# Kernel optimization log

Hardware: AMD Instinct MI355X
Metric: run time of the kernel (lower is better)

Reference implementation:

```python
import jax, jax.numpy as jnp
import numpy as np

N_NODES = 50000
N_EDGES = 1600000
NUM_MP_STEPS = 6


def _init_linear(key, d_in, d_out):
    kw, kb = jax.random.split(key)
    lim = 1.0 / np.sqrt(d_in)
    W = jax.random.uniform(kw, (d_in, d_out), jnp.float32, -lim, lim)
    b = jax.random.uniform(kb, (d_out,), jnp.float32, -lim, lim)
    return W, b


def setup_inputs() -> dict:
    key = jax.random.key(0)
    ks = jax.random.split(key, 12)
    inp = {
        'x': jax.random.normal(ks[0], (N_NODES, 32), jnp.float32),
        'edge_index': jax.random.randint(ks[1], (2, N_EDGES), 0, N_NODES, jnp.int64),
        'edge_attr': jax.random.normal(ks[2], (N_EDGES, 6), jnp.float32),
    }
    # encoder edge MLP: 6 -> 18 -> 18 -> 16 (leaky relu after every layer)
    inp['enc_W0'], inp['enc_b0'] = _init_linear(ks[3], 6, 18)
    inp['enc_W1'], inp['enc_b1'] = _init_linear(ks[4], 18, 18)
    inp['enc_W2'], inp['enc_b2'] = _init_linear(ks[5], 18, 16)
    # edge model MLP: 160 -> 80 -> 16 (leaky relu)
    inp['edge_W0'], inp['edge_b0'] = _init_linear(ks[6], 160, 80)
    inp['edge_W1'], inp['edge_b1'] = _init_linear(ks[7], 80, 16)
    # node model MLP: 80 -> 56 -> 32 (plain relu: MPGraph does not pass use_leaky_relu here)
    inp['node_W0'], inp['node_b0'] = _init_linear(ks[8], 80, 56)
    inp['node_W1'], inp['node_b1'] = _init_linear(ks[9], 56, 32)
    return inp


def reference(x, edge_index, edge_attr,
              enc_W0, enc_b0, enc_W1, enc_b1, enc_W2, enc_b2,
              edge_W0, edge_b0, edge_W1, edge_b1,
              node_W0, node_b0, node_W1, node_b1):
    lrelu = jax.nn.leaky_relu  # negative_slope=0.01, matches nn.LeakyReLU()
    relu = jax.nn.relu
    row, col = edge_index[0], edge_index[1]
    n_nodes = x.shape[0]

    # encoder on edge feats, LeakyReLU on node feats
    e = lrelu(lrelu(lrelu(edge_attr @ enc_W0 + enc_b0) @ enc_W1 + enc_b1) @ enc_W2 + enc_b2)
    n = lrelu(x)
    e0, n0 = e, n

    ones_e = jnp.ones((row.shape[0], 1), x.dtype)
    outputs = []
    for step in range(1, NUM_MP_STEPS + 1):
        ec = jnp.concatenate([e0, e], axis=1)            # [E, 32] reattach initial edges
        nc = jnp.concatenate([n0, n], axis=1)            # [N, 64] reattach initial nodes
        # edge update: gather endpoints, concat, MLP
        eh = jnp.concatenate([nc[row], nc[col], ec], axis=1)   # [E, 160]
        e = lrelu(lrelu(eh @ edge_W0 + edge_b0) @ edge_W1 + edge_b1)  # [E, 16]
        # node update: scatter-mean messages to source nodes, concat, MLP
        s = jax.ops.segment_sum(e, row, num_segments=n_nodes)         # [N, 16]
        cnt = jax.ops.segment_sum(ones_e, row, num_segments=n_nodes)  # [N, 1]
        msg = s / jnp.maximum(cnt, 1.0)
        nh = jnp.concatenate([nc, msg], axis=1)                        # [N, 80]
        n = relu(relu(nh @ node_W0 + node_b0) @ node_W1 + node_b1)     # [N, 32]
        if step > 1:
            outputs.append(e)
    return tuple(outputs)
```

## Files before the change

### kernel.cpp

```cpp
#include <hip/hip_runtime.h>

#define N_NODES 50000
#define N_EDGES 1600000

#define O_ENCW0 0
#define O_ENCB0 108
#define O_ENCW1 126
#define O_ENCB1 450
#define O_ENCW2 468
#define O_ENCB2 756
#define O_EDGEW0 772
#define O_EDGEB0 13572
#define O_EDGEW1 13652
#define O_EDGEB1 14932
#define O_NODEW0 14948
#define O_NODEB0 19428
#define O_NODEW1 19484
#define O_NODEB1 21276
#define W_TOTAL 21308

typedef __attribute__((ext_vector_type(8))) short bf16x8;
typedef __attribute__((ext_vector_type(4))) short bf16x4;
typedef __attribute__((ext_vector_type(4))) float f32x4;

__device__ __forceinline__ float bf2f(unsigned int u) {
    return __uint_as_float(u << 16);
}
__device__ __forceinline__ unsigned short f2bf(float f) {
    unsigned int u = __float_as_uint(f);
    u += 0x7fffu + ((u >> 16) & 1u);
    return (unsigned short)(u >> 16);
}
__device__ __forceinline__ float lrelu(float x) { return x > 0.f ? x : 0.01f * x; }

__device__ __forceinline__ bf16x8 pack8(float4 a, float4 b) {
    bf16x8 r;
    r[0] = (short)f2bf(a.x); r[1] = (short)f2bf(a.y);
    r[2] = (short)f2bf(a.z); r[3] = (short)f2bf(a.w);
    r[4] = (short)f2bf(b.x); r[5] = (short)f2bf(b.y);
    r[6] = (short)f2bf(b.z); r[7] = (short)f2bf(b.w);
    return r;
}

struct WPack {
    const float* p[14];
    int off[15];
};

__global__ void detect_flags(const int* __restrict__ eidx, int* __restrict__ flags) {
    int t = threadIdx.x;
    int v = eidx[2 * t + 1];
    unsigned long long bi = __ballot(v != 0);
    if (t == 0) flags[0] = (bi == 0ull) ? 1 : 0;
}

__device__ __forceinline__ void load_rc(const int* eidx, int flag64, int e, int& r, int& c) {
    if (flag64) {
        const long long* e64 = (const long long*)eidx;
        r = (int)e64[e];
        c = (int)e64[N_EDGES + e];
    } else {
        r = eidx[e];
        c = eidx[N_EDGES + e];
    }
}
__device__ __forceinline__ int load_r(const int* eidx, int flag64, int e) {
    return flag64 ? (int)((const long long*)eidx)[e] : eidx[e];
}

__global__ void copy_w(WPack P, float* __restrict__ dst) {
    int a = blockIdx.x;
    const float* s = P.p[a];
    int n = P.off[a + 1] - P.off[a];
    float* d = dst + P.off[a];
    for (int i = threadIdx.x; i < n; i += 256) d[i] = s[i];
}

__global__ void build_wT(const float* __restrict__ w0,
                         const float* __restrict__ w1,
                         unsigned short* __restrict__ wT) {
    int t = blockIdx.x * 256 + threadIdx.x;
    if (t < 12800) {
        int col = t / 160, k = t % 160;
        wT[t] = f2bf(w0[k * 80 + col]);
    } else if (t < 14336) {
        int u = t - 12800;
        int col = u / 96, k = u % 96;
        wT[t] = (k < 80) ? f2bf(w1[k * 16 + col]) : (unsigned short)0;
    }
}

__global__ void __launch_bounds__(256) init_nodes(const float* __restrict__ x,
                                                  unsigned short* __restrict__ ncb,
                                                  int* __restrict__ cnti) {
    int i = blockIdx.x * 256 + threadIdx.x;
    if (i >= N_NODES) return;
    const float4* xin = (const float4*)(x + (size_t)i * 32);
    uint4* np = (uint4*)(ncb + (size_t)i * 64);
#pragma unroll
    for (int q = 0; q < 4; q++) {
        float4 a = xin[2 * q];
        float4 b = xin[2 * q + 1];
        unsigned int w0 = (unsigned int)f2bf(lrelu(a.x)) | ((unsigned int)f2bf(lrelu(a.y)) << 16);
        unsigned int w1 = (unsigned int)f2bf(lrelu(a.z)) | ((unsigned int)f2bf(lrelu(a.w)) << 16);
        unsigned int w2 = (unsigned int)f2bf(lrelu(b.x)) | ((unsigned int)f2bf(lrelu(b.y)) << 16);
        unsigned int w3 = (unsigned int)f2bf(lrelu(b.z)) | ((unsigned int)f2bf(lrelu(b.w)) << 16);
        uint4 o = make_uint4(w0, w1, w2, w3);
        np[q] = o;
        np[4 + q] = o;
    }
    cnti[i] = 0;
}

__global__ void count_edges(const int* __restrict__ eidx, const int* __restrict__ flags,
                            int* __restrict__ cnti) {
    int e = blockIdx.x * 256 + threadIdx.x;
    atomicAdd(&cnti[load_r(eidx, flags[0], e)], 1);
}

__global__ void __launch_bounds__(256) scan_offsets(const int* __restrict__ cnti,
                                                    int* __restrict__ off,
                                                    int* __restrict__ cursor) {
    __shared__ int ls[256];
    const int t = threadIdx.x;
    const int lo = t * 196;
    const int hi = min(lo + 196, N_NODES);
    int sum = 0;
    for (int i = lo; i < hi; i++) sum += cnti[i];
    ls[t] = sum;
    __syncthreads();
    for (int d = 1; d < 256; d <<= 1) {
        int v = (t >= d) ? ls[t - d] : 0;
        __syncthreads();
        ls[t] += v;
        __syncthreads();
    }
    int run = (t == 0) ? 0 : ls[t - 1];
    for (int i = lo; i < hi; i++) {
        off[i] = run;
        cursor[i] = run;
        run += cnti[i];
    }
    if (t == 255) off[N_NODES] = run;
}

template <int EXT>
__global__ void build_perm(const int* __restrict__ eidx, const int* __restrict__ flags,
                           int* __restrict__ cursor, int* __restrict__ perm,
                           int2* __restrict__ rcp, int* __restrict__ pose) {
    int e = blockIdx.x * 256 + threadIdx.x;
    int r, c;
    load_rc(eidx, flags[0], e, r, c);
    int pos = atomicAdd(&cursor[r], 1);
    perm[pos] = e;
    if (EXT) {
        rcp[pos] = make_int2(r, c);
        pose[e] = pos;
    }
}

template <int MODE>
__global__ void __launch_bounds__(256) encoder(const float* __restrict__ ea,
                                               const float* __restrict__ wsW,
                                               float* __restrict__ outbase,
                                               unsigned short* __restrict__ e0b,
                                               const int* __restrict__ pose) {
    int e = blockIdx.x * 256 + threadIdx.x;
    const float* ap = ea + (size_t)e * 6;
    float a[6];
#pragma unroll
    for (int k = 0; k < 6; k++) a[k] = ap[k];

    float h1[18];
#pragma unroll
    for (int j = 0; j < 18; j++) h1[j] = wsW[O_ENCB0 + j];
#pragma unroll
    for (int k = 0; k < 6; k++) {
        float v = a[k];
#pragma unroll
        for (int j = 0; j < 18; j++) h1[j] = fmaf(v, wsW[O_ENCW0 + k * 18 + j], h1[j]);
    }
#pragma unroll
    for (int j = 0; j < 18; j++) h1[j] = lrelu(h1[j]);

    float h2[18];
#pragma unroll
    for (int j = 0; j < 18; j++) h2[j] = wsW[O_ENCB1 + j];
#pragma unroll
    for (int k = 0; k < 18; k++) {
        float v = h1[k];
#pragma unroll
        for (int j = 0; j < 18; j++) h2[j] = fmaf(v, wsW[O_ENCW1 + k * 18 + j], h2[j]);
    }
#pragma unroll
    for (int j = 0; j < 18; j++) h2[j] = lrelu(h2[j]);

    float o[16];
#pragma unroll
    for (int j = 0; j < 16; j++) o[j] = wsW[O_ENCB2 + j];
#pragma unroll
    for (int k = 0; k < 18; k++) {
        float v = h2[k];
#pragma unroll
        for (int j = 0; j < 16; j++) o[j] = fmaf(v, wsW[O_ENCW2 + k * 16 + j], o[j]);
    }
    if (MODE == 0) {
        float4* ow = (float4*)(outbase + (size_t)4 * N_EDGES * 16 + (size_t)e * 16);
#pragma unroll
        for (int q = 0; q < 4; q++)
            ow[q] = make_float4(lrelu(o[4 * q]), lrelu(o[4 * q + 1]),
                                lrelu(o[4 * q + 2]), lrelu(o[4 * q + 3]));
    } else {
        unsigned int pw[8];
#pragma unroll
        for (int q = 0; q < 8; q++) {
            float a0 = lrelu(o[2 * q]), a1 = lrelu(o[2 * q + 1]);
            pw[q] = (unsigned int)f2bf(a0) | ((unsigned int)f2bf(a1) << 16);
        }
        size_t pos = (MODE == 2) ? (size_t)pose[e] : (size_t)e;
        uint4* ow = (uint4*)(e0b + pos * 16);
        ow[0] = make_uint4(pw[0], pw[1], pw[2], pw[3]);
        ow[1] = make_uint4(pw[4], pw[5], pw[6], pw[7]);
    }
}


__global__ void __launch_bounds__(256) edge_mfma(const unsigned short* __restrict__ ncb,
                                                 const float* __restrict__ outb_c,
                                                 int slot_e0, int slot_prev, int slot_cur,
                                                 const int* __restrict__ eidx,
                                                 const int* __restrict__ flags,
                                                 const float* __restrict__ wsW,
                                                 const unsigned short* __restrict__ wT,
                                                 float* __restrict__ outb) {
    __shared__ unsigned short act1[4][32 * 104];
    const int lane = threadIdx.x & 63;
    const int wave = threadIdx.x >> 6;
    const int r16 = lane & 15;
    const int g = lane >> 4;
    const int flag64 = flags[0];
    unsigned short* aw = act1[wave];

    const int ebase = blockIdx.x * 128 + wave * 32;
    const float* e0s = outb_c + (size_t)slot_e0 * N_EDGES * 16;
    const float* eps = outb_c + (size_t)slot_prev * N_EDGES * 16;

#pragma unroll
    for (int u = 0; u < 2; u++) {
        bf16x4 z4 = {0, 0, 0, 0};
        *(bf16x4*)&aw[(u * 16 + r16) * 104 + 80 + g * 4] = z4;
    }

    bf16x8 a[2][5];
#pragma unroll
    for (int u = 0; u < 2; u++) {
        const int el = ebase + u * 16 + r16;
        int r_el, c_el;
        load_rc(eidx, flag64, el, r_el, c_el);
        a[u][0] = *(const bf16x8*)(ncb + (size_t)r_el * 64 + g * 8);
        a[u][1] = *(const bf16x8*)(ncb + (size_t)r_el * 64 + 32 + g * 8);
        a[u][2] = *(const bf16x8*)(ncb + (size_t)c_el * 64 + g * 8);
        a[u][3] = *(const bf16x8*)(ncb + (size_t)c_el * 64 + 32 + g * 8);
        const float* src = (g < 2) ? e0s : eps;
        const float4* p = (const float4*)(src + (size_t)el * 16 + (g & 1) * 8);
        a[u][4] = pack8(p[0], p[1]);
    }

#pragma unroll
    for (int t = 0; t < 5; t++) {
        float bv = wsW[O_EDGEB0 + t * 16 + r16];
        f32x4 acc0 = {bv, bv, bv, bv};
        f32x4 acc1 = {bv, bv, bv, bv};
#pragma unroll
        for (int st = 0; st < 5; st++) {
            bf16x8 b = *(const bf16x8*)(wT + (t * 16 + r16) * 160 + st * 32 + g * 8);
            acc0 = __builtin_amdgcn_mfma_f32_16x16x32_bf16(a[0][st], b, acc0, 0, 0, 0);
            acc1 = __builtin_amdgcn_mfma_f32_16x16x32_bf16(a[1][st], b, acc1, 0, 0, 0);
        }
#pragma unroll
        for (int i = 0; i < 4; i++) {
            aw[(g * 4 + i) * 104 + t * 16 + r16]      = f2bf(lrelu(acc0[i]));
            aw[(16 + g * 4 + i) * 104 + t * 16 + r16] = f2bf(lrelu(acc1[i]));
        }
    }
    asm volatile("s_waitcnt lgkmcnt(0)" ::: "memory");
    __builtin_amdgcn_sched_barrier(0);

    float bv2 = wsW[O_EDGEB1 + r16];
    f32x4 acc20 = {bv2, bv2, bv2, bv2};
    f32x4 acc21 = {bv2, bv2, bv2, bv2};
#pragma unroll
    for (int st = 0; st < 3; st++) {
        bf16x8 b2 = *(const bf16x8*)(wT + 12800 + r16 * 96 + st * 32 + g * 8);
        bf16x8 a20 = *(const bf16x8*)&aw[r16 * 104 + st * 32 + g * 8];
        bf16x8 a21 = *(const bf16x8*)&aw[(16 + r16) * 104 + st * 32 + g * 8];
        acc20 = __builtin_amdgcn_mfma_f32_16x16x32_bf16(a20, b2, acc20, 0, 0, 0);
        acc21 = __builtin_amdgcn_mfma_f32_16x16x32_bf16(a21, b2, acc21, 0, 0, 0);
    }

    float* oc = outb + (size_t)slot_cur * N_EDGES * 16;
#pragma unroll
    for (int i = 0; i < 4; i++) {
        int eg0 = ebase + g * 4 + i;
        int eg1 = ebase + 16 + g * 4 + i;
        oc[(size_t)eg0 * 16 + r16] = lrelu(acc20[i]);
        oc[(size_t)eg1 * 16 + r16] = lrelu(acc21[i]);
    }
}

template <int WOUT>
__global__ void __launch_bounds__(256) edge_mfma_b16(const unsigned short* __restrict__ ncb,
                                                     const unsigned short* __restrict__ e0b,
                                                     const unsigned short* __restrict__ prevb,
                                                     unsigned short* __restrict__ curb,
                                                     const int* __restrict__ eidx,
                                                     const int* __restrict__ flags,
                                                     const float* __restrict__ wsW,
                                                     const unsigned short* __restrict__ wT,
                                                     float* __restrict__ oc) {
    __shared__ unsigned short act1[4][32 * 104];
    const int lane = threadIdx.x & 63;
    const int wave = threadIdx.x >> 6;
    const int r16 = lane & 15;
    const int g = lane >> 4;
    const int flag64 = flags[0];
    unsigned short* aw = act1[wave];

    const int ebase = blockIdx.x * 128 + wave * 32;

#pragma unroll
    for (int u = 0; u < 2; u++) {
        bf16x4 z4 = {0, 0, 0, 0};
        *(bf16x4*)&aw[(u * 16 + r16) * 104 + 80 + g * 4] = z4;
    }

    bf16x8 a[2][5];
#pragma unroll
    for (int u = 0; u < 2; u++) {
        const int el = ebase + u * 16 + r16;
        int r_el, c_el;
        load_rc(eidx, flag64, el, r_el, c_el);
        a[u][0] = *(const bf16x8*)(ncb + (size_t)r_el * 64 + g * 8);
        a[u][1] = *(const bf16x8*)(ncb + (size_t)r_el * 64 + 32 + g * 8);
        a[u][2] = *(const bf16x8*)(ncb + (size_t)c_el * 64 + g * 8);
        a[u][3] = *(const bf16x8*)(ncb + (size_t)c_el * 64 + 32 + g * 8);
        const unsigned short* src = (g < 2) ? e0b : prevb;
        a[u][4] = *(const bf16x8*)(src + (size_t)el * 16 + (g & 1) * 8);
    }

#pragma unroll
    for (int t = 0; t < 5; t++) {
        float bv = wsW[O_EDGEB0 + t * 16 + r16];
        f32x4 acc0 = {bv, bv, bv, bv};
        f32x4 acc1 = {bv, bv, bv, bv};
#pragma unroll
        for (int st = 0; st < 5; st++) {
            bf16x8 b = *(const bf16x8*)(wT + (t * 16 + r16) * 160 + st * 32 + g * 8);
            acc0 = __builtin_amdgcn_mfma_f32_16x16x32_bf16(a[0][st], b, acc0, 0, 0, 0);
            acc1 = __builtin_amdgcn_mfma_f32_16x16x32_bf16(a[1][st], b, acc1, 0, 0, 0);
        }
#pragma unroll
        for (int i = 0; i < 4; i++) {
            aw[(g * 4 + i) * 104 + t * 16 + r16]      = f2bf(lrelu(acc0[i]));
            aw[(16 + g * 4 + i) * 104 + t * 16 + r16] = f2bf(lrelu(acc1[i]));
        }
    }
    asm volatile("s_waitcnt lgkmcnt(0)" ::: "memory");
    __builtin_amdgcn_sched_barrier(0);

    float bv2 = wsW[O_EDGEB1 + r16];
    f32x4 acc20 = {bv2, bv2, bv2, bv2};
    f32x4 acc21 = {bv2, bv2, bv2, bv2};
#pragma unroll
    for (int st = 0; st < 3; st++) {
        bf16x8 b2 = *(const bf16x8*)(wT + 12800 + r16 * 96 + st * 32 + g * 8);
        bf16x8 a20 = *(const bf16x8*)&aw[r16 * 104 + st * 32 + g * 8];
        bf16x8 a21 = *(const bf16x8*)&aw[(16 + r16) * 104 + st * 32 + g * 8];
        acc20 = __builtin_amdgcn_mfma_f32_16x16x32_bf16(a20, b2, acc20, 0, 0, 0);
        acc21 = __builtin_amdgcn_mfma_f32_16x16x32_bf16(a21, b2, acc21, 0, 0, 0);
    }

#pragma unroll
    for (int i = 0; i < 4; i++) {
        int eg0 = ebase + g * 4 + i;
        int eg1 = ebase + 16 + g * 4 + i;
        float v0 = lrelu(acc20[i]);
        float v1 = lrelu(acc21[i]);
        curb[(size_t)eg0 * 16 + r16] = f2bf(v0);
        curb[(size_t)eg1 * 16 + r16] = f2bf(v1);
        if (WOUT) {
            oc[(size_t)eg0 * 16 + r16] = v0;
            oc[(size_t)eg1 * 16 + r16] = v1;
        }
    }
}

template <int WOUT>
__global__ void __launch_bounds__(256) edge_mfma_perm(const unsigned short* __restrict__ ncb,
                                                      const unsigned short* __restrict__ e0b,
                                                      const unsigned short* __restrict__ prevb,
                                                      unsigned short* __restrict__ curb,
                                                      const int2* __restrict__ rcp,
                                                      const int* __restrict__ perm,
                                                      const float* __restrict__ wsW,
                                                      const unsigned short* __restrict__ wT,
                                                      float* __restrict__ oc) {
    __shared__ unsigned short act1[4][32 * 104];
    const int lane = threadIdx.x & 63;
    const int wave = threadIdx.x >> 6;
    const int r16 = lane & 15;
    const int g = lane >> 4;
    unsigned short* aw = act1[wave];

    const int pbase = blockIdx.x * 128 + wave * 32;

#pragma unroll
    for (int u = 0; u < 2; u++) {
        bf16x4 z4 = {0, 0, 0, 0};
        *(bf16x4*)&aw[(u * 16 + r16) * 104 + 80 + g * 4] = z4;
    }

    bf16x8 a[2][5];
#pragma unroll
    for (int u = 0; u < 2; u++) {
        const int pl = pbase + u * 16 + r16;
        int2 rc = rcp[pl];
        a[u][0] = *(const bf16x8*)(ncb + (size_t)rc.x * 64 + g * 8);
        a[u][1] = *(const bf16x8*)(ncb + (size_t)rc.x * 64 + 32 + g * 8);
        a[u][2] = *(const bf16x8*)(ncb + (size_t)rc.y * 64 + g * 8);
        a[u][3] = *(const bf16x8*)(ncb + (size_t)rc.y * 64 + 32 + g * 8);
        const unsigned short* src = (g < 2) ? e0b : prevb;
        a[u][4] = *(const bf16x8*)(src + (size_t)pl * 16 + (g & 1) * 8);
    }

#pragma unroll
    for (int t = 0; t < 5; t++) {
        float bv = wsW[O_EDGEB0 + t * 16 + r16];
        f32x4 acc0 = {bv, bv, bv, bv};
        f32x4 acc1 = {bv, bv, bv, bv};
#pragma unroll
        for (int st = 0; st < 5; st++) {
            bf16x8 b = *(const bf16x8*)(wT + (t * 16 + r16) * 160 + st * 32 + g * 8);
            acc0 = __builtin_amdgcn_mfma_f32_16x16x32_bf16(a[0][st], b, acc0, 0, 0, 0);
            acc1 = __builtin_amdgcn_mfma_f32_16x16x32_bf16(a[1][st], b, acc1, 0, 0, 0);
        }
#pragma unroll
        for (int i = 0; i < 4; i++) {
            aw[(g * 4 + i) * 104 + t * 16 + r16]      = f2bf(lrelu(acc0[i]));
            aw[(16 + g * 4 + i) * 104 + t * 16 + r16] = f2bf(lrelu(acc1[i]));
        }
    }
    asm volatile("s_waitcnt lgkmcnt(0)" ::: "memory");
    __builtin_amdgcn_sched_barrier(0);

    float bv2 = wsW[O_EDGEB1 + r16];
    f32x4 acc20 = {bv2, bv2, bv2, bv2};
    f32x4 acc21 = {bv2, bv2, bv2, bv2};
#pragma unroll
    for (int st = 0; st < 3; st++) {
        bf16x8 b2 = *(const bf16x8*)(wT + 12800 + r16 * 96 + st * 32 + g * 8);
        bf16x8 a20 = *(const bf16x8*)&aw[r16 * 104 + st * 32 + g * 8];
        bf16x8 a21 = *(const bf16x8*)&aw[(16 + r16) * 104 + st * 32 + g * 8];
        acc20 = __builtin_amdgcn_mfma_f32_16x16x32_bf16(a20, b2, acc20, 0, 0, 0);
        acc21 = __builtin_amdgcn_mfma_f32_16x16x32_bf16(a21, b2, acc21, 0, 0, 0);
    }

#pragma unroll
    for (int i = 0; i < 4; i++) {
        int p0l = pbase + g * 4 + i;
        int p1l = pbase + 16 + g * 4 + i;
        float v0 = lrelu(acc20[i]);
        float v1 = lrelu(acc21[i]);
        curb[(size_t)p0l * 16 + r16] = f2bf(v0);
        curb[(size_t)p1l * 16 + r16] = f2bf(v1);
        if (WOUT) {
            int eo0 = perm[p0l];
            int eo1 = perm[p1l];
            oc[(size_t)eo0 * 16 + r16] = v0;
            oc[(size_t)eo1 * 16 + r16] = v1;
        }
    }
}

__global__ void __launch_bounds__(256) gather_mean(const int* __restrict__ off,
                                                   const int* __restrict__ perm,
                                                   const float* __restrict__ ecur,
                                                   float* __restrict__ msg) {
    const int wave = threadIdx.x >> 6;
    const int lane = threadIdx.x & 63;
    const int i = blockIdx.x * 4 + wave;
    const int c = lane & 15;
    const int sub = lane >> 4;
    const int p0 = off[i], p1 = off[i + 1];
    float sum = 0.f;
    for (int p = p0 + sub; p < p1; p += 4)
        sum += ecur[(size_t)perm[p] * 16 + c];
    sum += __shfl_xor(sum, 16, 64);
    sum += __shfl_xor(sum, 32, 64);
    if (lane < 16) {
        float inv = 1.0f / fmaxf((float)(p1 - p0), 1.0f);
        msg[(size_t)i * 16 + c] = sum * inv;
    }
}

__global__ void __launch_bounds__(256) gather_mean_b16(const int* __restrict__ off,
                                                       const int* __restrict__ perm,
                                                       const unsigned short* __restrict__ ecurb,
                                                       float* __restrict__ msg) {
    const int wave = threadIdx.x >> 6;
    const int lane = threadIdx.x & 63;
    const int i = blockIdx.x * 4 + wave;
    const int c = lane & 15;
    const int sub = lane >> 4;
    const int p0 = off[i], p1 = off[i + 1];
    float sum = 0.f;
    for (int p = p0 + sub; p < p1; p += 4)
        sum += bf2f((unsigned int)ecurb[(size_t)perm[p] * 16 + c]);
    sum += __shfl_xor(sum, 16, 64);
    sum += __shfl_xor(sum, 32, 64);
    if (lane < 16) {
        float inv = 1.0f / fmaxf((float)(p1 - p0), 1.0f);
        msg[(size_t)i * 16 + c] = sum * inv;
    }
}

__global__ void __launch_bounds__(256) gather_mean_seq(const int* __restrict__ off,
                                                       const unsigned short* __restrict__ ecurb,
                                                       float* __restrict__ msg) {
    const int wave = threadIdx.x >> 6;
    const int lane = threadIdx.x & 63;
    const int i = blockIdx.x * 4 + wave;
    const int c = lane & 15;
    const int sub = lane >> 4;
    const int p0 = off[i], p1 = off[i + 1];
    float sum = 0.f;
    for (int p = p0 + sub; p < p1; p += 4)
        sum += bf2f((unsigned int)ecurb[(size_t)p * 16 + c]);
    sum += __shfl_xor(sum, 16, 64);
    sum += __shfl_xor(sum, 32, 64);
    if (lane < 16) {
        float inv = 1.0f / fmaxf((float)(p1 - p0), 1.0f);
        msg[(size_t)i * 16 + c] = sum * inv;
    }
}

__global__ void __launch_bounds__(64) node_mlp(const float* __restrict__ msg,
                                               unsigned short* __restrict__ ncb,
                                               const float* __restrict__ wsW) {
    __shared__ float sl[64 * 81];
    const int l = threadIdx.x;
    const int i = blockIdx.x * 64 + l;
    if (i >= N_NODES) return;
    const float* W0 = wsW + O_NODEW0;
    const float* b0 = wsW + O_NODEB0;
    const float* W1 = wsW + O_NODEW1;
    const float* b1 = wsW + O_NODEB1;

    const uint4* ncp = (const uint4*)(ncb + (size_t)i * 64);
#pragma unroll
    for (int q = 0; q < 8; q++) {
        uint4 u = ncp[q];
        int base = l * 81 + 8 * q;
        sl[base + 0] = bf2f(u.x & 0xffffu); sl[base + 1] = bf2f(u.x >> 16);
        sl[base + 2] = bf2f(u.y & 0xffffu); sl[base + 3] = bf2f(u.y >> 16);
        sl[base + 4] = bf2f(u.z & 0xffffu); sl[base + 5] = bf2f(u.z >> 16);
        sl[base + 6] = bf2f(u.w & 0xffffu); sl[base + 7] = bf2f(u.w >> 16);
    }
    const float4* mp = (const float4*)(msg + (size_t)i * 16);
#pragma unroll
    for (int q = 0; q < 4; q++) {
        float4 v = mp[q];
        int base = l * 81 + 64 + 4 * q;
        sl[base] = v.x; sl[base + 1] = v.y; sl[base + 2] = v.z; sl[base + 3] = v.w;
    }

    float h[56];
#pragma unroll
    for (int q = 0; q < 14; q++) {
        float4 b = ((const float4*)b0)[q];
        h[4 * q] = b.x; h[4 * q + 1] = b.y; h[4 * q + 2] = b.z; h[4 * q + 3] = b.w;
    }
    for (int k = 0; k < 80; k++) {
        float v = sl[l * 81 + k];
        const float4* w = (const float4*)(W0 + k * 56);
#pragma unroll
        for (int q = 0; q < 14; q++) {
            float4 wv = w[q];
            h[4 * q]     = fmaf(v, wv.x, h[4 * q]);
            h[4 * q + 1] = fmaf(v, wv.y, h[4 * q + 1]);
            h[4 * q + 2] = fmaf(v, wv.z, h[4 * q + 2]);
            h[4 * q + 3] = fmaf(v, wv.w, h[4 * q + 3]);
        }
    }
#pragma unroll
    for (int j = 0; j < 56; j++) sl[l * 81 + j] = fmaxf(h[j], 0.f);

    float o[32];
#pragma unroll
    for (int q = 0; q < 8; q++) {
        float4 b = ((const float4*)b1)[q];
        o[4 * q] = b.x; o[4 * q + 1] = b.y; o[4 * q + 2] = b.z; o[4 * q + 3] = b.w;
    }
    for (int j = 0; j < 56; j++) {
        float v = sl[l * 81 + j];
        const float4* w = (const float4*)(W1 + j * 32);
#pragma unroll
        for (int q = 0; q < 8; q++) {
            float4 wv = w[q];
            o[4 * q]     = fmaf(v, wv.x, o[4 * q]);
            o[4 * q + 1] = fmaf(v, wv.y, o[4 * q + 1]);
            o[4 * q + 2] = fmaf(v, wv.z, o[4 * q + 2]);
            o[4 * q + 3] = fmaf(v, wv.w, o[4 * q + 3]);
        }
    }
    uint4* nout = (uint4*)(ncb + (size_t)i * 64 + 32);
#pragma unroll
    for (int q = 0; q < 4; q++) {
        unsigned int w0 = (unsigned int)f2bf(fmaxf(o[8 * q + 0], 0.f)) |
                          ((unsigned int)f2bf(fmaxf(o[8 * q + 1], 0.f)) << 16);
        unsigned int w1 = (unsigned int)f2bf(fmaxf(o[8 * q + 2], 0.f)) |
                          ((unsigned int)f2bf(fmaxf(o[8 * q + 3], 0.f)) << 16);
        unsigned int w2 = (unsigned int)f2bf(fmaxf(o[8 * q + 4], 0.f)) |
                          ((unsigned int)f2bf(fmaxf(o[8 * q + 5], 0.f)) << 16);
        unsigned int w3 = (unsigned int)f2bf(fmaxf(o[8 * q + 6], 0.f)) |
                          ((unsigned int)f2bf(fmaxf(o[8 * q + 7], 0.f)) << 16);
        nout[q] = make_uint4(w0, w1, w2, w3);
    }
}

extern "C" void kernel_launch(void* const* d_in, const int* in_sizes, int n_in,
                              void* d_out, int out_size, void* d_ws, size_t ws_size,
                              hipStream_t stream) {
    (void)in_sizes; (void)n_in; (void)out_size;
    const float* x  = (const float*)d_in[0];
    const int* eidx = (const int*)d_in[1];
    const float* ea = (const float*)d_in[2];
    float* out = (float*)d_out;

    char* wsb = (char*)d_ws;
    float* wsW  = (float*)(wsb + 0);
    int* flags  = (int*)(wsb + 85232);
    int* cnti   = (int*)(wsb + 85248);
    int* off    = (int*)(wsb + 285248);
    int* cursor = (int*)(wsb + 485264);
    int* perm   = (int*)(wsb + 685264);
    unsigned short* ncb = (unsigned short*)(wsb + 7085264);
    unsigned short* wT  = (unsigned short*)(wsb + 13485264);
    float* msg  = (float*)(wsb + 13513936);
    const size_t WS_BASE = 16713936ull;
    unsigned short* e0b = (unsigned short*)(wsb + 16714240);
    unsigned short* rb0 = e0b + (size_t)N_EDGES * 16;
    unsigned short* rb1 = rb0 + (size_t)N_EDGES * 16;
    const size_t WS_BIG = 16714240ull + 3ull * 51200000ull;
    int2* rcp = (int2*)(wsb + 170314240ull);
    int* pose = (int*)(wsb + 183114240ull);
    const size_t WS_PERM = 189514240ull;
    if (ws_size < WS_BASE) return;
    const bool big  = (ws_size >= WS_BIG);
    const bool prm  = (ws_size >= WS_PERM);

    WPack P;
    static const int offs[15] = {0, 108, 126, 450, 468, 756, 772, 13572, 13652,
                                 14932, 14948, 19428, 19484, 21276, 21308};
    for (int a = 0; a < 14; a++) P.p[a] = (const float*)d_in[3 + a];
    for (int a = 0; a < 15; a++) P.off[a] = offs[a];

    detect_flags<<<1, 64, 0, stream>>>(eidx, flags);
    copy_w<<<14, 256, 0, stream>>>(P, wsW);
    build_wT<<<56, 256, 0, stream>>>((const float*)d_in[9], (const float*)d_in[11], wT);
    init_nodes<<<196, 256, 0, stream>>>(x, ncb, cnti);
    count_edges<<<N_EDGES / 256, 256, 0, stream>>>(eidx, flags, cnti);
    scan_offsets<<<1, 256, 0, stream>>>(cnti, off, cursor);
    if (prm)
        build_perm<1><<<N_EDGES / 256, 256, 0, stream>>>(eidx, flags, cursor, perm, rcp, pose);
    else
        build_perm<0><<<N_EDGES / 256, 256, 0, stream>>>(eidx, flags, cursor, perm, nullptr, nullptr);

    if (prm) {
        encoder<2><<<N_EDGES / 256, 256, 0, stream>>>(ea, wsW, out, e0b, pose);
        unsigned short* rings[2] = {rb0, rb1};
        for (int t = 1; t <= 6; t++) {
            unsigned short* prevb = (t == 1) ? e0b : rings[(t - 1) & 1];
            unsigned short* curb  = rings[t & 1];
            if (t == 1)
                edge_mfma_perm<0><<<N_EDGES / 128, 256, 0, stream>>>(
                    ncb, e0b, prevb, curb, rcp, perm, wsW, wT, out);
            else
                edge_mfma_perm<1><<<N_EDGES / 128, 256, 0, stream>>>(
                    ncb, e0b, prevb, curb, rcp, perm, wsW, wT,
                    out + (size_t)(t - 2) * N_EDGES * 16);
            if (t < 6) {
                gather_mean_seq<<<12500, 256, 0, stream>>>(off, curb, msg);
                node_mlp<<<782, 64, 0, stream>>>(msg, ncb, wsW);
            }
        }
    } else if (big) {
        encoder<1><<<N_EDGES / 256, 256, 0, stream>>>(ea, wsW, out, e0b, nullptr);
        unsigned short* rings[2] = {rb0, rb1};
        for (int t = 1; t <= 6; t++) {
            unsigned short* prevb = (t == 1) ? e0b : rings[(t - 1) & 1];
            unsigned short* curb  = rings[t & 1];
            if (t == 1)
                edge_mfma_b16<0><<<N_EDGES / 128, 256, 0, stream>>>(
                    ncb, e0b, prevb, curb, eidx, flags, wsW, wT, out);
            else
                edge_mfma_b16<1><<<N_EDGES / 128, 256, 0, stream>>>(
                    ncb, e0b, prevb, curb, eidx, flags, wsW, wT,
                    out + (size_t)(t - 2) * N_EDGES * 16);
            if (t < 6) {
                gather_mean_b16<<<12500, 256, 0, stream>>>(off, perm, curb, msg);
                node_mlp<<<782, 64, 0, stream>>>(msg, ncb, wsW);
            }
        }
    } else {
        encoder<0><<<N_EDGES / 256, 256, 0, stream>>>(ea, wsW, out, nullptr, nullptr);
        const int prevs[6] = {4, 0, 0, 1, 2, 3};
        const int curs[6]  = {0, 0, 1, 2, 3, 4};
        for (int t = 1; t <= 6; t++) {
            edge_mfma<<<N_EDGES / 128, 256, 0, stream>>>(ncb, out, 4, prevs[t - 1],
                                                         curs[t - 1], eidx, flags, wsW,
                                                         wT, out);
            if (t < 6) {
                gather_mean<<<12500, 256, 0, stream>>>(
                    off, perm, out + (size_t)curs[t - 1] * N_EDGES * 16, msg);
                node_mlp<<<782, 64, 0, stream>>>(msg, ncb, wsW);
            }
        }
    }
}
```

Measured before the change: 1.604 ms.

## Fuse segment-mean gather with node MLP using bf16 MFMA per 16-node wave tile

Replaces the separate gather_mean_seq and scalar node_mlp kernels with one node_fused kernel. Each wave gathers 16 nodes' features and mean messages into LDS, then runs both node MLP layers with 16x16x32 bf16 MFMA against pre-transposed, padded node weights built once by a new build_wnT kernel. This removes a launch and the fp32 msg round trip and moves the node MLP onto matrix cores. In exchange the gather is serialized per node within each wave, so fewer waves are in flight, and layer inputs and outputs are rounded to bf16. The wn buffer reuses the msg workspace region.

```diff
diff --git a/kernel.cpp b/kernel.cpp
--- a/kernel.cpp
+++ b/kernel.cpp
@@ -87,6 +87,19 @@
         int u = t - 12800;
         int col = u / 96, k = u % 96;
         wT[t] = (k < 80) ? f2bf(w1[k * 16 + col]) : (unsigned short)0;
+    }
+}
+
+__global__ void build_wnT(const float* __restrict__ nw0, const float* __restrict__ nw1,
+                          unsigned short* __restrict__ wn) {
+    int t = blockIdx.x * 256 + threadIdx.x;
+    if (t < 6144) {
+        int col = t / 96, k = t % 96;
+        wn[t] = (col < 56 && k < 80) ? f2bf(nw0[k * 56 + col]) : (unsigned short)0;
+    } else if (t < 8192) {
+        int u = t - 6144;
+        int col = u / 64, k = u % 64;
+        wn[t] = (k < 56) ? f2bf(nw1[k * 32 + col]) : (unsigned short)0;
     }
 }
 
@@ -524,26 +537,6 @@
     }
 }
 
-__global__ void __launch_bounds__(256) gather_mean_seq(const int* __restrict__ off,
-                                                       const unsigned short* __restrict__ ecurb,
-                                                       float* __restrict__ msg) {
-    const int wave = threadIdx.x >> 6;
-    const int lane = threadIdx.x & 63;
-    const int i = blockIdx.x * 4 + wave;
-    const int c = lane & 15;
-    const int sub = lane >> 4;
-    const int p0 = off[i], p1 = off[i + 1];
-    float sum = 0.f;
-    for (int p = p0 + sub; p < p1; p += 4)
-        sum += bf2f((unsigned int)ecurb[(size_t)p * 16 + c]);
-    sum += __shfl_xor(sum, 16, 64);
-    sum += __shfl_xor(sum, 32, 64);
-    if (lane < 16) {
-        float inv = 1.0f / fmaxf((float)(p1 - p0), 1.0f);
-        msg[(size_t)i * 16 + c] = sum * inv;
-    }
-}
-
 __global__ void __launch_bounds__(64) node_mlp(const float* __restrict__ msg,
                                                unsigned short* __restrict__ ncb,
                                                const float* __restrict__ wsW) {
@@ -628,6 +621,85 @@
     }
 }
 
+__global__ void __launch_bounds__(256) node_fused(const int* __restrict__ off,
+                                                  const unsigned short* __restrict__ ecurb,
+                                                  unsigned short* __restrict__ ncb,
+                                                  const float* __restrict__ wsW,
+                                                  const unsigned short* __restrict__ wn) {
+    __shared__ unsigned short nhs[4][16 * 104];
+    __shared__ unsigned short act2[4][16 * 72];
+    const int lane = threadIdx.x & 63;
+    const int wave = threadIdx.x >> 6;
+    const int r16 = lane & 15;
+    const int g = lane >> 4;
+    unsigned short* nh = nhs[wave];
+    unsigned short* a2w = act2[wave];
+    const int n0 = blockIdx.x * 64 + wave * 16;
+
+    {
+        int i = lane >> 2, q = lane & 3;
+        int node = n0 + i; if (node >= N_NODES) node = 0;
+        const uint4* src = (const uint4*)(ncb + (size_t)node * 64 + q * 16);
+        uint4 v0 = src[0], v1 = src[1];
+        *(uint4*)&nh[i * 104 + q * 16] = v0;
+        *(uint4*)&nh[i * 104 + q * 16 + 8] = v1;
+        bf16x4 z4 = {0, 0, 0, 0};
+        *(bf16x4*)&nh[i * 104 + 80 + q * 4] = z4;
+    }
+
+    for (int i = 0; i < 16; i++) {
+        int node = n0 + i;
+        int nodeC = (node < N_NODES) ? node : 0;
+        int p0 = off[nodeC], p1 = off[nodeC + 1];
+        float sum = 0.f;
+        for (int p = p0 + g; p < p1; p += 4)
+            sum += bf2f((unsigned int)ecurb[(size_t)p * 16 + r16]);
+        sum += __shfl_xor(sum, 16, 64);
+        sum += __shfl_xor(sum, 32, 64);
+        if (lane < 16) {
+            float inv = 1.0f / fmaxf((float)(p1 - p0), 1.0f);
+            nh[i * 104 + 64 + r16] = f2bf(sum * inv);
+        }
+    }
+    asm volatile("s_waitcnt lgkmcnt(0)" ::: "memory");
+    __builtin_amdgcn_sched_barrier(0);
+
+#pragma unroll
+    for (int t = 0; t < 4; t++) {
+        float bv = wsW[O_NODEB0 + t * 16 + r16];
+        f32x4 acc = {bv, bv, bv, bv};
+#pragma unroll
+        for (int st = 0; st < 3; st++) {
+            bf16x8 av = *(const bf16x8*)&nh[r16 * 104 + st * 32 + g * 8];
+            bf16x8 bw = *(const bf16x8*)(wn + (t * 16 + r16) * 96 + st * 32 + g * 8);
+            acc = __builtin_amdgcn_mfma_f32_16x16x32_bf16(av, bw, acc, 0, 0, 0);
+        }
+#pragma unroll
+        for (int i = 0; i < 4; i++)
+            a2w[(g * 4 + i) * 72 + t * 16 + r16] = f2bf(fmaxf(acc[i], 0.f));
+    }
+    asm volatile("s_waitcnt lgkmcnt(0)" ::: "memory");
+    __builtin_amdgcn_sched_barrier(0);
+
+#pragma unroll
+    for (int t2 = 0; t2 < 2; t2++) {
+        float bv = wsW[O_NODEB1 + t2 * 16 + r16];
+        f32x4 acc = {bv, bv, bv, bv};
+#pragma unroll
+        for (int st = 0; st < 2; st++) {
+            bf16x8 av = *(const bf16x8*)&a2w[r16 * 72 + st * 32 + g * 8];
+            bf16x8 bw = *(const bf16x8*)(wn + 6144 + (t2 * 16 + r16) * 64 + st * 32 + g * 8);
+            acc = __builtin_amdgcn_mfma_f32_16x16x32_bf16(av, bw, acc, 0, 0, 0);
+        }
+#pragma unroll
+        for (int i = 0; i < 4; i++) {
+            int node = n0 + g * 4 + i;
+            if (node < N_NODES)
+                ncb[(size_t)node * 64 + 32 + t2 * 16 + r16] = f2bf(fmaxf(acc[i], 0.f));
+        }
+    }
+}
+
 extern "C" void kernel_launch(void* const* d_in, const int* in_sizes, int n_in,
                               void* d_out, int out_size, void* d_ws, size_t ws_size,
                               hipStream_t stream) {
@@ -647,6 +719,7 @@
     unsigned short* ncb = (unsigned short*)(wsb + 7085264);
     unsigned short* wT  = (unsigned short*)(wsb + 13485264);
     float* msg  = (float*)(wsb + 13513936);
+    unsigned short* wn = (unsigned short*)(wsb + 13513936);
     const size_t WS_BASE = 16713936ull;
     unsigned short* e0b = (unsigned short*)(wsb + 16714240);
     unsigned short* rb0 = e0b + (size_t)N_EDGES * 16;
@@ -677,6 +750,7 @@
         build_perm<0><<<N_EDGES / 256, 256, 0, stream>>>(eidx, flags, cursor, perm, nullptr, nullptr);
 
     if (prm) {
+        build_wnT<<<32, 256, 0, stream>>>((const float*)d_in[13], (const float*)d_in[15], wn);
         encoder<2><<<N_EDGES / 256, 256, 0, stream>>>(ea, wsW, out, e0b, pose);
         unsigned short* rings[2] = {rb0, rb1};
         for (int t = 1; t <= 6; t++) {
@@ -689,10 +763,8 @@
                 edge_mfma_perm<1><<<N_EDGES / 128, 256, 0, stream>>>(
                     ncb, e0b, prevb, curb, rcp, perm, wsW, wT,
                     out + (size_t)(t - 2) * N_EDGES * 16);
-            if (t < 6) {
-                gather_mean_seq<<<12500, 256, 0, stream>>>(off, curb, msg);
-                node_mlp<<<782, 64, 0, stream>>>(msg, ncb, wsW);
-            }
+            if (t < 6)
+                node_fused<<<782, 256, 0, stream>>>(off, curb, ncb, wsW, wn);
         }
     } else if (big) {
         encoder<1><<<N_EDGES / 256, 256, 0, stream>>>(ea, wsW, out, e0b, nullptr);
```

After: 1.567 ms. -2.3%, faster.
